# Kernel tuning notes

Hardware: AMD Instinct MI355X
Metric: run time of the kernel (lower is better)

Reference implementation:

```python
import jax, jax.numpy as jnp
import numpy as np

S_DIM = 1024      # sequence_state_dim
INNER = 32        # inner_dim
PAIR = 128        # pairwise_state_dim
EPS = 1e-5


def setup_inputs() -> dict:
    key = jax.random.key(0)
    ks = jax.random.split(key, 6)
    B, L = 1, 1024
    sequence_state = jax.random.normal(ks[0], (B, L, S_DIM), dtype=jnp.float32)
    # LayerNorm params
    ln_gamma = jnp.ones((S_DIM,), dtype=jnp.float32)
    ln_beta = jnp.zeros((S_DIM,), dtype=jnp.float32)
    # proj: Linear(S_DIM -> 2*INNER), bias initialized to zeros in the module
    proj_w = jax.random.normal(ks[1], (S_DIM, 2 * INNER), dtype=jnp.float32) / np.sqrt(S_DIM)
    proj_b = jnp.zeros((2 * INNER,), dtype=jnp.float32)
    # o_proj: Linear(2*INNER -> PAIR), bias zeros
    o_w = jax.random.normal(ks[2], (2 * INNER, PAIR), dtype=jnp.float32) / np.sqrt(2 * INNER)
    o_b = jnp.zeros((PAIR,), dtype=jnp.float32)
    return {
        "sequence_state": sequence_state,
        "ln_gamma": ln_gamma,
        "ln_beta": ln_beta,
        "proj_w": proj_w,
        "proj_b": proj_b,
        "o_w": o_w,
        "o_b": o_b,
    }


def reference(sequence_state, ln_gamma, ln_beta, proj_w, proj_b, o_w, o_b):
    # LayerNorm over last dim
    mu = jnp.mean(sequence_state, axis=-1, keepdims=True)
    var = jnp.mean(jnp.square(sequence_state - mu), axis=-1, keepdims=True)
    s = (sequence_state - mu) * jax.lax.rsqrt(var + EPS) * ln_gamma + ln_beta
    # proj to q, k  [B, L, INNER] each
    s = jnp.einsum("bld,dh->blh", s, proj_w) + proj_b
    q, k = s[..., :INNER], s[..., INNER:]
    # pair features: prod[b,i,j,c] = q[b,j,c]*k[b,i,c]; diff = q[b,j,c]-k[b,i,c]
    prod = q[:, None, :, :] * k[:, :, None, :]   # [B, L, L, INNER]
    diff = q[:, None, :, :] - k[:, :, None, :]   # [B, L, L, INNER]
    x = jnp.concatenate([prod, diff], axis=-1)   # [B, L, L, 2*INNER]
    return jnp.einsum("bijc,cp->bijp", x, o_w) + o_b  # [B, L, L, PAIR]
```

## Files before the change

kernel.cpp:

```cpp
#include <hip/hip_runtime.h>
#include <hip/hip_bf16.h>

#define S_DIM 1024
#define INNER 32
#define PAIR  128
#define LSEQ  1024

__global__ __launch_bounds__(256) void ln_proj_kernel(
    const float* __restrict__ x,
    const float* __restrict__ gamma,
    const float* __restrict__ beta,
    const float* __restrict__ pw,
    const float* __restrict__ pb,
    const float* __restrict__ ow,
    float* __restrict__ qk,
    float* __restrict__ Aq,
    float* __restrict__ Ak)
{
    const int row  = blockIdx.x;
    const int t    = threadIdx.x;
    const int lane = t & 63;
    const int wv   = t >> 6;

    __shared__ float s_sh[S_DIM];
    __shared__ float wsum[4], wsum2[4];
    __shared__ float hpart[4][64];
    __shared__ float h_sh[64];

    float4 xv = ((const float4*)(x + (size_t)row * S_DIM))[t];
    float sum = xv.x + xv.y + xv.z + xv.w;
    float sq  = xv.x*xv.x + xv.y*xv.y + xv.z*xv.z + xv.w*xv.w;
    #pragma unroll
    for (int off = 32; off; off >>= 1) {
        sum += __shfl_down(sum, off, 64);
        sq  += __shfl_down(sq,  off, 64);
    }
    if (lane == 0) { wsum[wv] = sum; wsum2[wv] = sq; }
    __syncthreads();
    float tot  = wsum[0] + wsum[1] + wsum[2] + wsum[3];
    float tot2 = wsum2[0] + wsum2[1] + wsum2[2] + wsum2[3];
    float mu   = tot * (1.0f / S_DIM);
    float var  = tot2 * (1.0f / S_DIM) - mu * mu;
    float rstd = rsqrtf(var + 1e-5f);

    float4 gv = ((const float4*)gamma)[t];
    float4 bv = ((const float4*)beta)[t];
    float4 sv;
    sv.x = (xv.x - mu) * rstd * gv.x + bv.x;
    sv.y = (xv.y - mu) * rstd * gv.y + bv.y;
    sv.z = (xv.z - mu) * rstd * gv.z + bv.z;
    sv.w = (xv.w - mu) * rstd * gv.w + bv.w;
    ((float4*)s_sh)[t] = sv;
    __syncthreads();

    {
        const int c    = lane;
        const int part = wv;
        const int dbase = part * 256;
        const float* pwp = pw + c;
        float acc = 0.f;
        for (int d = 0; d < 256; ++d) {
            acc = fmaf(s_sh[dbase + d], pwp[(size_t)(dbase + d) * 64], acc);
        }
        hpart[part][c] = acc;
    }
    __syncthreads();
    if (t < 64) {
        float h = hpart[0][t] + hpart[1][t] + hpart[2][t] + hpart[3][t] + pb[t];
        h_sh[t] = h;
        qk[(size_t)row * 64 + t] = h;
    }
    __syncthreads();

    {
        const int p    = t & 127;
        const int half = t >> 7;
        const float* w2 = ow + 32 * PAIR + p;
        const float* hh = h_sh + half * 32;
        float acc = 0.f;
        #pragma unroll
        for (int c = 0; c < 32; ++c)
            acc = fmaf(hh[c], w2[(size_t)c * PAIR], acc);
        if (half == 0) Aq[(size_t)row * PAIR + p] = acc;
        else           Ak[(size_t)row * PAIR + p] = acc;
    }
}

__global__ __launch_bounds__(256) void pair_kernel(
    const float* __restrict__ qk,
    const float* __restrict__ Aq,
    const float* __restrict__ Ak,
    const float* __restrict__ ow,
    const float* __restrict__ ob,
    float* __restrict__ out)
{
    const int i    = blockIdx.x;
    const int jblk = blockIdx.y;
    const int lane = threadIdx.x & 63;
    const int wv   = threadIdx.x >> 6;
    const int p0   = lane;
    const int p1   = lane + 64;

    float kw0[32], kw1[32];
    const float4* k4 = (const float4*)(qk + (size_t)i * 64 + 32);
    #pragma unroll
    for (int c4 = 0; c4 < 8; ++c4) {
        float4 kv = k4[c4];
        const float* w1 = ow + (size_t)(c4 * 4) * PAIR;
        kw0[c4*4+0] = kv.x * w1[0*PAIR + p0];
        kw1[c4*4+0] = kv.x * w1[0*PAIR + p1];
        kw0[c4*4+1] = kv.y * w1[1*PAIR + p0];
        kw1[c4*4+1] = kv.y * w1[1*PAIR + p1];
        kw0[c4*4+2] = kv.z * w1[2*PAIR + p0];
        kw1[c4*4+2] = kv.z * w1[2*PAIR + p1];
        kw0[c4*4+3] = kv.w * w1[3*PAIR + p0];
        kw1[c4*4+3] = kv.w * w1[3*PAIR + p1];
    }

    const float bias0 = ob[p0] - Ak[(size_t)i * PAIR + p0];
    const float bias1 = ob[p1] - Ak[(size_t)i * PAIR + p1];

    const int jbase = jblk * 128 + wv * 32;
    for (int jj = 0; jj < 32; ++jj) {
        int j = __builtin_amdgcn_readfirstlane(jbase + jj);
        const float4* q4 = (const float4*)(qk + (size_t)j * 64);
        float a0 = bias0 + Aq[(size_t)j * PAIR + p0];
        float a1 = bias1 + Aq[(size_t)j * PAIR + p1];
        #pragma unroll
        for (int c4 = 0; c4 < 8; ++c4) {
            float4 qv = q4[c4];
            a0 = fmaf(qv.x, kw0[c4*4+0], a0);
            a1 = fmaf(qv.x, kw1[c4*4+0], a1);
            a0 = fmaf(qv.y, kw0[c4*4+1], a0);
            a1 = fmaf(qv.y, kw1[c4*4+1], a1);
            a0 = fmaf(qv.z, kw0[c4*4+2], a0);
            a1 = fmaf(qv.z, kw1[c4*4+2], a1);
            a0 = fmaf(qv.w, kw0[c4*4+3], a0);
            a1 = fmaf(qv.w, kw1[c4*4+3], a1);
        }
        size_t off = ((size_t)i * LSEQ + (size_t)j) * PAIR;
        out[off + p0] = a0;
        out[off + p1] = a1;
    }
}

extern "C" void kernel_launch(void* const* d_in, const int* in_sizes, int n_in,
                              void* d_out, int out_size, void* d_ws, size_t ws_size,
                              hipStream_t stream) {
    const float* x     = (const float*)d_in[0];
    const float* gamma = (const float*)d_in[1];
    const float* beta  = (const float*)d_in[2];
    const float* pw    = (const float*)d_in[3];
    const float* pb    = (const float*)d_in[4];
    const float* ow    = (const float*)d_in[5];
    const float* ob    = (const float*)d_in[6];
    float* out = (float*)d_out;

    float* qk = (float*)d_ws;
    float* Aq = qk + (size_t)LSEQ * 64;
    float* Ak = Aq + (size_t)LSEQ * PAIR;

    ln_proj_kernel<<<dim3(LSEQ), dim3(256), 0, stream>>>(
        x, gamma, beta, pw, pb, ow, qk, Aq, Ak);

    pair_kernel<<<dim3(LSEQ, 8), dim3(256), 0, stream>>>(
        qk, Aq, Ak, ow, ob, out);
}
```

Baseline: 631.8 us.

## Vectorize pair kernel to float2 lanes, process two j rows, nontemporal stores

```diff
diff --git a/kernel.cpp b/kernel.cpp
--- a/kernel.cpp
+++ b/kernel.cpp
@@ -5,6 +5,8 @@
 #define INNER 32
 #define PAIR  128
 #define LSEQ  1024
+
+typedef float f2 __attribute__((ext_vector_type(2)));
 
 __global__ __launch_bounds__(256) void ln_proj_kernel(
     const float* __restrict__ x,
@@ -59,6 +61,7 @@
         const int dbase = part * 256;
         const float* pwp = pw + c;
         float acc = 0.f;
+        #pragma unroll 8
         for (int d = 0; d < 256; ++d) {
             acc = fmaf(s_sh[dbase + d], pwp[(size_t)(dbase + d) * 64], acc);
         }
@@ -98,49 +101,65 @@
     const int jblk = blockIdx.y;
     const int lane = threadIdx.x & 63;
     const int wv   = threadIdx.x >> 6;
-    const int p0   = lane;
-    const int p1   = lane + 64;
 
-    float kw0[32], kw1[32];
-    const float4* k4 = (const float4*)(qk + (size_t)i * 64 + 32);
-    #pragma unroll
-    for (int c4 = 0; c4 < 8; ++c4) {
-        float4 kv = k4[c4];
-        const float* w1 = ow + (size_t)(c4 * 4) * PAIR;
-        kw0[c4*4+0] = kv.x * w1[0*PAIR + p0];
-        kw1[c4*4+0] = kv.x * w1[0*PAIR + p1];
-        kw0[c4*4+1] = kv.y * w1[1*PAIR + p0];
-        kw1[c4*4+1] = kv.y * w1[1*PAIR + p1];
-        kw0[c4*4+2] = kv.z * w1[2*PAIR + p0];
-        kw1[c4*4+2] = kv.z * w1[2*PAIR + p1];
-        kw0[c4*4+3] = kv.w * w1[3*PAIR + p0];
-        kw1[c4*4+3] = kv.w * w1[3*PAIR + p1];
+    f2 kw[32];
+    {
+        const float4* k4 = (const float4*)(qk + (size_t)i * 64 + 32);
+        #pragma unroll
+        for (int c4 = 0; c4 < 8; ++c4) {
+            float4 kv = k4[c4];
+            const f2* w1a = (const f2*)(ow + (size_t)(c4*4+0) * PAIR);
+            const f2* w1b = (const f2*)(ow + (size_t)(c4*4+1) * PAIR);
+            const f2* w1c = (const f2*)(ow + (size_t)(c4*4+2) * PAIR);
+            const f2* w1d = (const f2*)(ow + (size_t)(c4*4+3) * PAIR);
+            kw[c4*4+0] = kv.x * w1a[lane];
+            kw[c4*4+1] = kv.y * w1b[lane];
+            kw[c4*4+2] = kv.z * w1c[lane];
+            kw[c4*4+3] = kv.w * w1d[lane];
+        }
     }
 
-    const float bias0 = ob[p0] - Ak[(size_t)i * PAIR + p0];
-    const float bias1 = ob[p1] - Ak[(size_t)i * PAIR + p1];
+    const f2 bias = ((const f2*)ob)[lane] - ((const f2*)(Ak + (size_t)i * PAIR))[lane];
+    const f2* Aq2 = (const f2*)Aq;
+    f2* out2 = (f2*)out;
 
     const int jbase = jblk * 128 + wv * 32;
-    for (int jj = 0; jj < 32; ++jj) {
-        int j = __builtin_amdgcn_readfirstlane(jbase + jj);
-        const float4* q4 = (const float4*)(qk + (size_t)j * 64);
-        float a0 = bias0 + Aq[(size_t)j * PAIR + p0];
-        float a1 = bias1 + Aq[(size_t)j * PAIR + p1];
+    #pragma unroll 2
+    for (int jj = 0; jj < 32; jj += 2) {
+        const int j0 = __builtin_amdgcn_readfirstlane(jbase + jj);
+        const int j1 = j0 + 1;
+        const float4* q40 = (const float4*)(qk + (size_t)j0 * 64);
+        const float4* q41 = (const float4*)(qk + (size_t)j1 * 64);
+
+        f2 a0 = bias + Aq2[(size_t)j0 * 64 + lane];
+        f2 a1 = bias + Aq2[(size_t)j1 * 64 + lane];
+        f2 b0 = {0.f, 0.f};
+        f2 b1 = {0.f, 0.f};
+
         #pragma unroll
-        for (int c4 = 0; c4 < 8; ++c4) {
-            float4 qv = q4[c4];
-            a0 = fmaf(qv.x, kw0[c4*4+0], a0);
-            a1 = fmaf(qv.x, kw1[c4*4+0], a1);
-            a0 = fmaf(qv.y, kw0[c4*4+1], a0);
-            a1 = fmaf(qv.y, kw1[c4*4+1], a1);
-            a0 = fmaf(qv.z, kw0[c4*4+2], a0);
-            a1 = fmaf(qv.z, kw1[c4*4+2], a1);
-            a0 = fmaf(qv.w, kw0[c4*4+3], a0);
-            a1 = fmaf(qv.w, kw1[c4*4+3], a1);
+        for (int c4 = 0; c4 < 4; ++c4) {
+            float4 qv0 = q40[c4];
+            float4 qv1 = q41[c4];
+            a0 += qv0.x * kw[c4*4+0];  a1 += qv1.x * kw[c4*4+0];
+            a0 += qv0.y * kw[c4*4+1];  a1 += qv1.y * kw[c4*4+1];
+            a0 += qv0.z * kw[c4*4+2];  a1 += qv1.z * kw[c4*4+2];
+            a0 += qv0.w * kw[c4*4+3];  a1 += qv1.w * kw[c4*4+3];
         }
-        size_t off = ((size_t)i * LSEQ + (size_t)j) * PAIR;
-        out[off + p0] = a0;
-        out[off + p1] = a1;
+        #pragma unroll
+        for (int c4 = 4; c4 < 8; ++c4) {
+            float4 qv0 = q40[c4];
+            float4 qv1 = q41[c4];
+            b0 += qv0.x * kw[c4*4+0];  b1 += qv1.x * kw[c4*4+0];
+            b0 += qv0.y * kw[c4*4+1];  b1 += qv1.y * kw[c4*4+1];
+            b0 += qv0.z * kw[c4*4+2];  b1 += qv1.z * kw[c4*4+2];
+            b0 += qv0.w * kw[c4*4+3];  b1 += qv1.w * kw[c4*4+3];
+        }
+        a0 += b0;
+        a1 += b1;
+
+        const size_t off0 = ((size_t)i * LSEQ + (size_t)j0) * (PAIR / 2);
+        __builtin_nontemporal_store(a0, out2 + off0 + lane);
+        __builtin_nontemporal_store(a1, out2 + off0 + 64 + lane);
     }
 }
 
```

After: 569.7 us. 9.8% less time.

## Vectorize pair kernel with float4 stores and double-buffered q prefetch

Applied to the files above, without the earlier changes.

```diff
diff --git a/kernel.cpp b/kernel.cpp
--- a/kernel.cpp
+++ b/kernel.cpp
@@ -1,10 +1,11 @@
 #include <hip/hip_runtime.h>
-#include <hip/hip_bf16.h>
 
 #define S_DIM 1024
 #define INNER 32
 #define PAIR  128
 #define LSEQ  1024
+
+typedef float f4 __attribute__((ext_vector_type(4)));
 
 __global__ __launch_bounds__(256) void ln_proj_kernel(
     const float* __restrict__ x,
@@ -59,6 +60,7 @@
         const int dbase = part * 256;
         const float* pwp = pw + c;
         float acc = 0.f;
+        #pragma unroll 8
         for (int d = 0; d < 256; ++d) {
             acc = fmaf(s_sh[dbase + d], pwp[(size_t)(dbase + d) * 64], acc);
         }
@@ -86,7 +88,7 @@
     }
 }
 
-__global__ __launch_bounds__(256) void pair_kernel(
+__global__ __launch_bounds__(256, 2) void pair_kernel(
     const float* __restrict__ qk,
     const float* __restrict__ Aq,
     const float* __restrict__ Ak,
@@ -98,49 +100,78 @@
     const int jblk = blockIdx.y;
     const int lane = threadIdx.x & 63;
     const int wv   = threadIdx.x >> 6;
-    const int p0   = lane;
-    const int p1   = lane + 64;
+    const int h    = lane >> 5;
+    const int pl   = lane & 31;
 
-    float kw0[32], kw1[32];
-    const float4* k4 = (const float4*)(qk + (size_t)i * 64 + 32);
-    #pragma unroll
-    for (int c4 = 0; c4 < 8; ++c4) {
-        float4 kv = k4[c4];
-        const float* w1 = ow + (size_t)(c4 * 4) * PAIR;
-        kw0[c4*4+0] = kv.x * w1[0*PAIR + p0];
-        kw1[c4*4+0] = kv.x * w1[0*PAIR + p1];
-        kw0[c4*4+1] = kv.y * w1[1*PAIR + p0];
-        kw1[c4*4+1] = kv.y * w1[1*PAIR + p1];
-        kw0[c4*4+2] = kv.z * w1[2*PAIR + p0];
-        kw1[c4*4+2] = kv.z * w1[2*PAIR + p1];
-        kw0[c4*4+3] = kv.w * w1[3*PAIR + p0];
-        kw1[c4*4+3] = kv.w * w1[3*PAIR + p1];
+    f4 kw4[32];
+    {
+        const float4* kvp = (const float4*)(qk + (size_t)i * 64 + 32);
+        #pragma unroll
+        for (int c4 = 0; c4 < 8; ++c4) {
+            float4 kv = kvp[c4];
+            const f4* wa = (const f4*)(ow + (size_t)(c4*4+0) * PAIR) + pl;
+            const f4* wb = (const f4*)(ow + (size_t)(c4*4+1) * PAIR) + pl;
+            const f4* wc = (const f4*)(ow + (size_t)(c4*4+2) * PAIR) + pl;
+            const f4* wd = (const f4*)(ow + (size_t)(c4*4+3) * PAIR) + pl;
+            kw4[c4*4+0] = kv.x * wa[0];
+            kw4[c4*4+1] = kv.y * wb[0];
+            kw4[c4*4+2] = kv.z * wc[0];
+            kw4[c4*4+3] = kv.w * wd[0];
+        }
     }
 
-    const float bias0 = ob[p0] - Ak[(size_t)i * PAIR + p0];
-    const float bias1 = ob[p1] - Ak[(size_t)i * PAIR + p1];
+    const f4 bias = ((const f4*)ob)[pl] - ((const f4*)(Ak + (size_t)i * PAIR))[pl];
 
-    const int jbase = jblk * 128 + wv * 32;
-    for (int jj = 0; jj < 32; ++jj) {
-        int j = __builtin_amdgcn_readfirstlane(jbase + jj);
-        const float4* q4 = (const float4*)(qk + (size_t)j * 64);
-        float a0 = bias0 + Aq[(size_t)j * PAIR + p0];
-        float a1 = bias1 + Aq[(size_t)j * PAIR + p1];
-        #pragma unroll
-        for (int c4 = 0; c4 < 8; ++c4) {
-            float4 qv = q4[c4];
-            a0 = fmaf(qv.x, kw0[c4*4+0], a0);
-            a1 = fmaf(qv.x, kw1[c4*4+0], a1);
-            a0 = fmaf(qv.y, kw0[c4*4+1], a0);
-            a1 = fmaf(qv.y, kw1[c4*4+1], a1);
-            a0 = fmaf(qv.z, kw0[c4*4+2], a0);
-            a1 = fmaf(qv.z, kw1[c4*4+2], a1);
-            a0 = fmaf(qv.w, kw0[c4*4+3], a0);
-            a1 = fmaf(qv.w, kw1[c4*4+3], a1);
+    const int j0 = __builtin_amdgcn_readfirstlane(jblk * 128 + wv * 32);
+
+    const f4* qp  = (const f4*)(qk + (size_t)(j0 + h) * 64);
+    const f4* aqp = (const f4*)Aq + ((size_t)(j0 + h) * 32 + pl);
+    f4*       op  = (f4*)out + (((size_t)i * LSEQ + (j0 + h)) * 32 + pl);
+
+    f4 qA[8], qB[8], aqA, aqB;
+    #pragma unroll
+    for (int c4 = 0; c4 < 8; ++c4) qA[c4] = qp[c4];
+    aqA = aqp[0];
+    #pragma unroll
+    for (int c4 = 0; c4 < 8; ++c4) qB[c4] = qp[32 + c4];
+    aqB = aqp[64];
+
+    #pragma unroll 1
+    for (int t = 0; t < 16; t += 2) {
+        {
+            f4 acc0 = bias + aqA;
+            f4 acc1 = {0.f, 0.f, 0.f, 0.f};
+            #pragma unroll
+            for (int c4 = 0; c4 < 4; ++c4) {
+                f4 qv = qA[c4];
+                f4 qw = qA[c4 + 4];
+                acc0 += qv.x * kw4[c4*4+0];   acc1 += qw.x * kw4[16 + c4*4+0];
+                acc0 += qv.y * kw4[c4*4+1];   acc1 += qw.y * kw4[16 + c4*4+1];
+                acc0 += qv.z * kw4[c4*4+2];   acc1 += qw.z * kw4[16 + c4*4+2];
+                acc0 += qv.w * kw4[c4*4+3];   acc1 += qw.w * kw4[16 + c4*4+3];
+            }
+            #pragma unroll
+            for (int c4 = 0; c4 < 8; ++c4) qA[c4] = qp[(size_t)(t + 2) * 32 + c4];
+            aqA = aqp[(size_t)(t + 2) * 64];
+            op[(size_t)t * 64] = acc0 + acc1;
         }
-        size_t off = ((size_t)i * LSEQ + (size_t)j) * PAIR;
-        out[off + p0] = a0;
-        out[off + p1] = a1;
+        {
+            f4 acc0 = bias + aqB;
+            f4 acc1 = {0.f, 0.f, 0.f, 0.f};
+            #pragma unroll
+            for (int c4 = 0; c4 < 4; ++c4) {
+                f4 qv = qB[c4];
+                f4 qw = qB[c4 + 4];
+                acc0 += qv.x * kw4[c4*4+0];   acc1 += qw.x * kw4[16 + c4*4+0];
+                acc0 += qv.y * kw4[c4*4+1];   acc1 += qw.y * kw4[16 + c4*4+1];
+                acc0 += qv.z * kw4[c4*4+2];   acc1 += qw.z * kw4[16 + c4*4+2];
+                acc0 += qv.w * kw4[c4*4+3];   acc1 += qw.w * kw4[16 + c4*4+3];
+            }
+            #pragma unroll
+            for (int c4 = 0; c4 < 8; ++c4) qB[c4] = qp[(size_t)(t + 3) * 32 + c4];
+            aqB = aqp[(size_t)(t + 3) * 64];
+            op[(size_t)(t + 1) * 64] = acc0 + acc1;
+        }
     }
 }
 
```

Result: slower. 901.6 us (+42.7%).
